# Performance work log

Hardware: AMD Instinct MI355X
Metric: run time of the kernel (lower is better)

Reference implementation:

```python
import jax, jax.numpy as jnp
import numpy as np

NIN, DIM, NHEAD = 512, 64, 8
B, N = 2, 2048

def setup_inputs() -> dict:
    key = jax.random.key(0)
    ks = jax.random.split(key, 7)
    s = 1.0 / np.sqrt(NIN)  # torch Linear default init range
    out_f = DIM * NHEAD
    return {
        "x": jax.random.normal(ks[0], (B, N, NIN), dtype=jnp.float32),
        "Wq": jax.random.uniform(ks[1], (out_f, NIN), jnp.float32, -s, s),
        "bq": jax.random.uniform(ks[2], (out_f,), jnp.float32, -s, s),
        "Wk": jax.random.uniform(ks[3], (out_f, NIN), jnp.float32, -s, s),
        "bk": jax.random.uniform(ks[4], (out_f,), jnp.float32, -s, s),
        "Wv": jax.random.uniform(ks[5], (out_f, NIN), jnp.float32, -s, s),
        "bv": jax.random.uniform(ks[6], (out_f,), jnp.float32, -s, s),
    }

def reference(x, Wq, bq, Wk, bk, Wv, bv):
    b, n, nin = x.shape
    scale = DIM ** (-0.5)
    # torch: self.qs(x).view(nhead, B, N, dim) -- a FLAT reshape, not a transpose
    q = (x @ Wq.T + bq).reshape(NHEAD, b, n, DIM)
    k = (x @ Wk.T + bk).reshape(NHEAD, b, n, DIM)
    v = (x @ Wv.T + bv).reshape(NHEAD, b, n, DIM)
    # no softmax in the original module; mask path is a no-op (masked_fill not in-place)
    att = jnp.einsum('hbid,hbjd->hbij', q, k) * scale  # [h,b,n,n]
    out = jnp.einsum('hbij,hbjd->hbid', att, v)        # [h,b,n,d]
    out = jnp.transpose(out, (1, 2, 3, 0))             # [b,n,d,h]
    return out.reshape(b, n, -1)
```

## Files before the change

### kernel.cpp

```cpp
#include <hip/hip_runtime.h>
#include <stdint.h>

#define CHELEM 131072

typedef __attribute__((ext_vector_type(4))) float   f32x4;
typedef __attribute__((ext_vector_type(8))) short   bh8;
typedef __attribute__((ext_vector_type(4))) unsigned short u16x4;
typedef __attribute__((ext_vector_type(8))) unsigned short u16x8;
typedef unsigned short u16;

__device__ inline u16 f2bf(float f) {
    union { float f; uint32_t u; } v; v.f = f;
    uint32_t u = v.u;
    u += 0x7FFF + ((u >> 16) & 1);
    return (u16)(u >> 16);
}

__device__ inline uint32_t cvt2(float lo, float hi) {
    uint32_t r;
    asm("v_cvt_pk_bf16_f32 %0, %1, %2" : "=v"(r) : "v"(lo), "v"(hi));
    return r;
}

__global__ __launch_bounds__(256, 3) void k1_qkv(
        const float* __restrict__ x,
        const float* __restrict__ Wq, const float* __restrict__ Wk,
        const float* __restrict__ Wv,
        const float* __restrict__ bq, const float* __restrict__ bk,
        const float* __restrict__ bv,
        u16* __restrict__ Qb, u16* __restrict__ Kb, u16* __restrict__ Vb) {
    __shared__ u16 smem[2][12288];
    const int tid  = threadIdx.x;
    const int lane = tid & 63, wid = tid >> 6;
    const int wr = wid >> 1, wc = wid & 1;
    const int swz  = (blockIdx.x & 7) * 96 + (blockIdx.x >> 3);
    const int mb = swz / 12, nb = swz % 12;
    const int w    = nb >> 2;
    const int nloc = (nb & 3) * 128;
    const float4* x4 = (const float4*)x;
    const float4* W4 = (const float4*)((w == 0) ? Wq : ((w == 1) ? Wk : Wv));
    const float*  bias = (w == 0) ? bq : ((w == 1) ? bk : bv);
    u16*          out  = (w == 0) ? Qb : ((w == 1) ? Kb : Vb);
    const int m0 = mb * 64;

    f32x4 acc[2][4] = {};
    float4 ra[4], rb[8];

    auto issue = [&](int kb) {
        const int k4 = kb * 16;
#pragma unroll
        for (int v = 0; v < 4; ++v) {
            const int idx = v * 256 + tid;
            ra[v] = x4[(size_t)(m0 + (idx >> 4)) * 128 + k4 + (idx & 15)];
        }
#pragma unroll
        for (int v = 0; v < 8; ++v) {
            const int idx = v * 256 + tid;
            rb[v] = W4[(size_t)(nloc + (idx >> 4)) * 128 + k4 + (idx & 15)];
        }
    };
    auto cvt_write = [&](int b) {
        u16* bA = smem[b];
        u16* bB = smem[b] + 4096;
#pragma unroll
        for (int v = 0; v < 4; ++v) {
            const int idx = v * 256 + tid;
            uint32_t p0 = cvt2(ra[v].x, ra[v].y);
            uint32_t p1 = cvt2(ra[v].z, ra[v].w);
            uint2 pk; pk.x = p0; pk.y = p1;
            *(uint2*)&bA[(idx >> 4) * 64 + (idx & 15) * 4] = pk;
        }
#pragma unroll
        for (int v = 0; v < 8; ++v) {
            const int idx = v * 256 + tid;
            uint32_t p0 = cvt2(rb[v].x, rb[v].y);
            uint32_t p1 = cvt2(rb[v].z, rb[v].w);
            uint2 pk; pk.x = p0; pk.y = p1;
            *(uint2*)&bB[(idx >> 4) * 64 + (idx & 15) * 4] = pk;
        }
    };
    auto compute = [&](int b) {
        const u16* bA = smem[b];
        const u16* bB = smem[b] + 4096;
#pragma unroll
        for (int ks = 0; ks < 2; ++ks) {
            const int kk = ks * 32 + (lane >> 4) * 8;
            bh8 a[2], bfr[4];
#pragma unroll
            for (int i = 0; i < 2; ++i)
                a[i] = *(const bh8*)&bA[(wr * 32 + i * 16 + (lane & 15)) * 64 + kk];
#pragma unroll
            for (int j = 0; j < 4; ++j)
                bfr[j] = *(const bh8*)&bB[(wc * 64 + j * 16 + (lane & 15)) * 64 + kk];
#pragma unroll
            for (int i = 0; i < 2; ++i)
#pragma unroll
                for (int j = 0; j < 4; ++j)
                    acc[i][j] = __builtin_amdgcn_mfma_f32_16x16x32_bf16(a[i], bfr[j], acc[i][j], 0, 0, 0);
        }
    };

    issue(0);
    cvt_write(0);
    __syncthreads();
    for (int kb = 0; kb < 8; ++kb) {
        if (kb < 7) issue(kb + 1);
        compute(kb & 1);
        if (kb < 7) cvt_write((kb + 1) & 1);
        __syncthreads();
    }

    if (w == 0) {
#pragma unroll
        for (int i = 0; i < 2; ++i) {
            const int row_base = m0 + wr * 32 + i * 16 + ((lane >> 4) * 4);
#pragma unroll
            for (int j = 0; j < 4; ++j) {
                const int col = nloc + wc * 64 + j * 16 + (lane & 15);
                const float bv_ = bias[col];
#pragma unroll
                for (int r = 0; r < 4; ++r)
                    out[(size_t)(row_base + r) * 512 + col] = f2bf(acc[i][j][r] + bv_);
            }
        }
    } else {
        u16 (*tile)[130] = (u16(*)[130])smem;
#pragma unroll
        for (int i = 0; i < 2; ++i) {
            const int ml = wr * 32 + i * 16 + ((lane >> 4) * 4);
#pragma unroll
            for (int j = 0; j < 4; ++j) {
                const int nl = wc * 64 + j * 16 + (lane & 15);
                const float bv_ = bias[nloc + nl];
#pragma unroll
                for (int r = 0; r < 4; ++r)
                    tile[ml + r][nl] = f2bf(acc[i][j][r] + bv_);
            }
        }
        __syncthreads();
        const int ncol  = tid & 127;
        const int mhalf = tid >> 7;
        const int g = (nb & 3) * 2 + (ncol >> 6);
        const int d = ncol & 63;
        const int c = mb >> 2;
        const int qbase = (mb & 3) * 64 + mhalf * 32;
        u16* dst = out + (size_t)c * CHELEM + d * 2048 + g * 256 + qbase;
#pragma unroll
        for (int v = 0; v < 4; ++v) {
            u16x8 t;
#pragma unroll
            for (int j = 0; j < 8; ++j)
                t[j] = tile[mhalf * 32 + v * 8 + j][ncol];
            *(u16x8*)(dst + v * 8) = t;
        }
    }
}

__global__ __launch_bounds__(256) void k2_pmat(
        const u16* __restrict__ Kt2, const u16* __restrict__ Vt2,
        u16* __restrict__ Pb) {
    __shared__ float red[4][16][16];
    const int tid = threadIdx.x;
    const int lane = tid & 63, w = tid >> 6;
    const int c   = blockIdx.x & 15;
    const int sub = blockIdx.x >> 4;
    const int dq = sub >> 2, eq = sub & 3;
    const u16* Vc = Vt2 + (size_t)c * CHELEM;
    const u16* Kc = Kt2 + (size_t)c * CHELEM;
    const int krow = lane & 15;
    const int arow = (dq * 16 + krow) * 2048;
    const int brow = (eq * 16 + krow) * 2048;
    const int kb = w * 512 + (lane >> 4) * 8;

    f32x4 acc = {};
#pragma unroll
    for (int kt = 0; kt < 16; ++kt) {
        const int k0 = kb + kt * 32;
        bh8 a = *(const bh8*)&Vc[arow + k0];
        bh8 b = *(const bh8*)&Kc[brow + k0];
        acc = __builtin_amdgcn_mfma_f32_16x16x32_bf16(a, b, acc, 0, 0, 0);
    }
#pragma unroll
    for (int r = 0; r < 4; ++r)
        red[w][(lane >> 4) * 4 + r][lane & 15] = acc[r];
    __syncthreads();
    const int row = tid >> 4, col = tid & 15;
    float s = red[0][row][col] + red[1][row][col] + red[2][row][col] + red[3][row][col];
    Pb[c * 4096 + (dq * 16 + row) * 64 + eq * 16 + col] = f2bf(s * 0.125f);
}

__global__ __launch_bounds__(256) void k3_out(
        const u16* __restrict__ Qb, const u16* __restrict__ Pb,
        float* __restrict__ outp) {
    const int tid = threadIdx.x;
    const int lane = tid & 63, w = tid >> 6;
    const int bid = blockIdx.x;
    const int bb = bid >> 7;
    const int ib = bid & 127;
    const int i0 = ib * 16;
    const int dbase = w * 16;
    const int krow = lane & 15;
    const int koff = (lane >> 4) * 8;

    f32x4 acc[8] = {};
#pragma unroll
    for (int h = 0; h < 8; ++h) {
        const int c = h * 2 + bb;
        const u16* Qc = Qb + (size_t)c * CHELEM;
        const u16* Pc = Pb + c * 4096;
#pragma unroll
        for (int ks = 0; ks < 2; ++ks) {
            bh8 a = *(const bh8*)&Qc[(i0 + krow) * 64 + ks * 32 + koff];
            bh8 b = *(const bh8*)&Pc[(dbase + krow) * 64 + ks * 32 + koff];
            acc[h] = __builtin_amdgcn_mfma_f32_16x16x32_bf16(a, b, acc[h], 0, 0, 0);
        }
    }
    const int orow_base = bb * 2048 + i0 + (lane >> 4) * 4;
    const int d = dbase + (lane & 15);
#pragma unroll
    for (int r = 0; r < 4; ++r) {
        f32x4 lo = {acc[0][r], acc[1][r], acc[2][r], acc[3][r]};
        f32x4 hi = {acc[4][r], acc[5][r], acc[6][r], acc[7][r]};
        float* dst = outp + (size_t)(orow_base + r) * 512 + d * 8;
        *(f32x4*)dst = lo;
        *(f32x4*)(dst + 4) = hi;
    }
}

extern "C" void kernel_launch(void* const* d_in, const int* in_sizes, int n_in,
                              void* d_out, int out_size, void* d_ws, size_t ws_size,
                              hipStream_t stream) {
    const float* x  = (const float*)d_in[0];
    const float* Wq = (const float*)d_in[1];
    const float* bq = (const float*)d_in[2];
    const float* Wk = (const float*)d_in[3];
    const float* bk = (const float*)d_in[4];
    const float* Wv = (const float*)d_in[5];
    const float* bv = (const float*)d_in[6];
    float* outp = (float*)d_out;

    u16* Qb = (u16*)d_ws;
    u16* Kb = Qb + 2097152;
    u16* Vb = Kb + 2097152;
    u16* Pb = Vb + 2097152;

    k1_qkv<<<768, 256, 0, stream>>>(x, Wq, Wk, Wv, bq, bk, bv, Qb, Kb, Vb);
    k2_pmat<<<256, 256, 0, stream>>>(Kb, Vb, Pb);
    k3_out<<<256, 256, 0, stream>>>(Qb, Pb, outp);
}
```

Baseline: 37.80 us.

## Stage full x tile in swizzled LDS once; stream W directly into registers

The QKV projection kernel now loads the block's whole 64x512 x tile into LDS as bf16 once, using an XOR swizzle to avoid bank conflicts, before the K loop. W fragments are loaded straight from global memory into registers, converted to bf16 and double-buffered per K step, with no LDS staging. Each wave now owns 32 output columns across all 64 rows. This drops the per-iteration __syncthreads and the LDS round trip for W, at the cost of 64KB of LDS, which lowers occupancy to 2 blocks per CU, and less coalesced global loads for W.

```diff
diff --git a/kernel.cpp b/kernel.cpp
--- a/kernel.cpp
+++ b/kernel.cpp
@@ -22,101 +22,115 @@
     return r;
 }
 
-__global__ __launch_bounds__(256, 3) void k1_qkv(
+union U4B8 { uint4 u; bh8 b; };
+
+__global__ __launch_bounds__(256, 2) void k1_qkv(
         const float* __restrict__ x,
         const float* __restrict__ Wq, const float* __restrict__ Wk,
         const float* __restrict__ Wv,
         const float* __restrict__ bq, const float* __restrict__ bk,
         const float* __restrict__ bv,
         u16* __restrict__ Qb, u16* __restrict__ Kb, u16* __restrict__ Vb) {
-    __shared__ u16 smem[2][12288];
+    __shared__ u16 smem[32768];
     const int tid  = threadIdx.x;
-    const int lane = tid & 63, wid = tid >> 6;
-    const int wr = wid >> 1, wc = wid & 1;
+    const int lane = tid & 63;
+    const int w    = tid >> 6;
     const int swz  = (blockIdx.x & 7) * 96 + (blockIdx.x >> 3);
     const int mb = swz / 12, nb = swz % 12;
-    const int w    = nb >> 2;
+    const int wsel = nb >> 2;
     const int nloc = (nb & 3) * 128;
     const float4* x4 = (const float4*)x;
-    const float4* W4 = (const float4*)((w == 0) ? Wq : ((w == 1) ? Wk : Wv));
-    const float*  bias = (w == 0) ? bq : ((w == 1) ? bk : bv);
-    u16*          out  = (w == 0) ? Qb : ((w == 1) ? Kb : Vb);
+    const float4* W4 = (const float4*)((wsel == 0) ? Wq : ((wsel == 1) ? Wk : Wv));
+    const float*  bias = (wsel == 0) ? bq : ((wsel == 1) ? bk : bv);
+    u16*          out  = (wsel == 0) ? Qb : ((wsel == 1) ? Kb : Vb);
     const int m0 = mb * 64;
 
-    f32x4 acc[2][4] = {};
-    float4 ra[4], rb[8];
-
-    auto issue = [&](int kb) {
-        const int k4 = kb * 16;
-#pragma unroll
-        for (int v = 0; v < 4; ++v) {
-            const int idx = v * 256 + tid;
-            ra[v] = x4[(size_t)(m0 + (idx >> 4)) * 128 + k4 + (idx & 15)];
-        }
-#pragma unroll
-        for (int v = 0; v < 8; ++v) {
-            const int idx = v * 256 + tid;
-            rb[v] = W4[(size_t)(nloc + (idx >> 4)) * 128 + k4 + (idx & 15)];
-        }
+    const int browA = nloc + w * 32 + (lane & 15);
+    const int bk4   = (lane >> 4) * 2;
+    auto issueB = [&](int s, float4* rb) {
+#pragma unroll
+        for (int g = 0; g < 2; ++g)
+#pragma unroll
+            for (int ks = 0; ks < 2; ++ks)
+#pragma unroll
+                for (int h = 0; h < 2; ++h)
+                    rb[(g * 2 + ks) * 2 + h] =
+                        W4[(size_t)(browA + g * 16) * 128 + s * 16 + ks * 8 + bk4 + h];
     };
-    auto cvt_write = [&](int b) {
-        u16* bA = smem[b];
-        u16* bB = smem[b] + 4096;
-#pragma unroll
-        for (int v = 0; v < 4; ++v) {
-            const int idx = v * 256 + tid;
-            uint32_t p0 = cvt2(ra[v].x, ra[v].y);
-            uint32_t p1 = cvt2(ra[v].z, ra[v].w);
-            uint2 pk; pk.x = p0; pk.y = p1;
-            *(uint2*)&bA[(idx >> 4) * 64 + (idx & 15) * 4] = pk;
-        }
-#pragma unroll
-        for (int v = 0; v < 8; ++v) {
-            const int idx = v * 256 + tid;
-            uint32_t p0 = cvt2(rb[v].x, rb[v].y);
-            uint32_t p1 = cvt2(rb[v].z, rb[v].w);
-            uint2 pk; pk.x = p0; pk.y = p1;
-            *(uint2*)&bB[(idx >> 4) * 64 + (idx & 15) * 4] = pk;
+    auto cvtB = [&](const float4* rb, bh8* bfr) {
+#pragma unroll
+        for (int q = 0; q < 4; ++q) {
+            U4B8 t;
+            t.u.x = cvt2(rb[q * 2].x,     rb[q * 2].y);
+            t.u.y = cvt2(rb[q * 2].z,     rb[q * 2].w);
+            t.u.z = cvt2(rb[q * 2 + 1].x, rb[q * 2 + 1].y);
+            t.u.w = cvt2(rb[q * 2 + 1].z, rb[q * 2 + 1].w);
+            bfr[q] = t.b;
         }
     };
-    auto compute = [&](int b) {
-        const u16* bA = smem[b];
-        const u16* bB = smem[b] + 4096;
+
+    float4 rb0[8], rb1[8];
+    issueB(0, rb0);
+    {
+        float4 rx0[4], rx1[4];
+        auto issueA = [&](int b, float4* rx) {
+#pragma unroll
+            for (int v = 0; v < 4; ++v) {
+                const int idx = (b * 4 + v) * 256 + tid;
+                rx[v] = x4[(size_t)(m0 + (idx >> 7)) * 128 + (idx & 127)];
+            }
+        };
+        auto writeA = [&](int b, const float4* rx) {
+#pragma unroll
+            for (int v = 0; v < 4; ++v) {
+                const int idx = (b * 4 + v) * 256 + tid;
+                const int row = idx >> 7, c4 = idx & 127;
+                uint2 pk; pk.x = cvt2(rx[v].x, rx[v].y); pk.y = cvt2(rx[v].z, rx[v].w);
+                *(uint2*)((char*)smem + row * 1024 + ((c4 * 8) ^ ((row & 7) << 4))) = pk;
+            }
+        };
+        issueA(0, rx0);
+#pragma unroll
+        for (int b = 0; b < 8; ++b) {
+            if (b & 1) { if (b < 7) issueA(b + 1, rx0); writeA(b, rx1); }
+            else       { if (b < 7) issueA(b + 1, rx1); writeA(b, rx0); }
+        }
+    }
+    __syncthreads();
+
+    f32x4 acc[4][2] = {};
+    const int arow_l = lane & 15;
+    const int akoff  = (lane >> 4) * 8;
+#pragma unroll
+    for (int s = 0; s < 8; ++s) {
+        bh8 bfr[4];
+        if (s & 1) { if (s < 7) issueB(s + 1, rb0); cvtB(rb1, bfr); }
+        else       { if (s < 7) issueB(s + 1, rb1); cvtB(rb0, bfr); }
 #pragma unroll
         for (int ks = 0; ks < 2; ++ks) {
-            const int kk = ks * 32 + (lane >> 4) * 8;
-            bh8 a[2], bfr[4];
-#pragma unroll
-            for (int i = 0; i < 2; ++i)
-                a[i] = *(const bh8*)&bA[(wr * 32 + i * 16 + (lane & 15)) * 64 + kk];
-#pragma unroll
-            for (int j = 0; j < 4; ++j)
-                bfr[j] = *(const bh8*)&bB[(wc * 64 + j * 16 + (lane & 15)) * 64 + kk];
-#pragma unroll
-            for (int i = 0; i < 2; ++i)
-#pragma unroll
-                for (int j = 0; j < 4; ++j)
-                    acc[i][j] = __builtin_amdgcn_mfma_f32_16x16x32_bf16(a[i], bfr[j], acc[i][j], 0, 0, 0);
-        }
-    };
-
-    issue(0);
-    cvt_write(0);
-    __syncthreads();
-    for (int kb = 0; kb < 8; ++kb) {
-        if (kb < 7) issue(kb + 1);
-        compute(kb & 1);
-        if (kb < 7) cvt_write((kb + 1) & 1);
-        __syncthreads();
-    }
-
-    if (w == 0) {
-#pragma unroll
-        for (int i = 0; i < 2; ++i) {
-            const int row_base = m0 + wr * 32 + i * 16 + ((lane >> 4) * 4);
-#pragma unroll
-            for (int j = 0; j < 4; ++j) {
-                const int col = nloc + wc * 64 + j * 16 + (lane & 15);
+            bh8 aa[4];
+#pragma unroll
+            for (int i = 0; i < 4; ++i) {
+                const int row = i * 16 + arow_l;
+                const int kk2 = ((s * 64 + ks * 32 + akoff) * 2) ^ ((row & 7) << 4);
+                aa[i] = *(const bh8*)((const char*)smem + row * 1024 + kk2);
+            }
+#pragma unroll
+            for (int i = 0; i < 4; ++i)
+#pragma unroll
+                for (int j = 0; j < 2; ++j)
+                    acc[i][j] = __builtin_amdgcn_mfma_f32_16x16x32_bf16(
+                        aa[i], bfr[j * 2 + ks], acc[i][j], 0, 0, 0);
+        }
+    }
+
+    if (wsel == 0) {
+#pragma unroll
+        for (int i = 0; i < 4; ++i) {
+            const int row_base = m0 + i * 16 + ((lane >> 4) * 4);
+#pragma unroll
+            for (int j = 0; j < 2; ++j) {
+                const int col = nloc + w * 32 + j * 16 + (lane & 15);
                 const float bv_ = bias[col];
 #pragma unroll
                 for (int r = 0; r < 4; ++r)
@@ -124,13 +138,14 @@
             }
         }
     } else {
+        __syncthreads();
         u16 (*tile)[130] = (u16(*)[130])smem;
 #pragma unroll
-        for (int i = 0; i < 2; ++i) {
-            const int ml = wr * 32 + i * 16 + ((lane >> 4) * 4);
-#pragma unroll
-            for (int j = 0; j < 4; ++j) {
-                const int nl = wc * 64 + j * 16 + (lane & 15);
+        for (int i = 0; i < 4; ++i) {
+            const int ml = i * 16 + ((lane >> 4) * 4);
+#pragma unroll
+            for (int j = 0; j < 2; ++j) {
+                const int nl = w * 32 + j * 16 + (lane & 15);
                 const float bv_ = bias[nloc + nl];
 #pragma unroll
                 for (int r = 0; r < 4; ++r)
```

Result: slower. 55.77 us (+47.6%).
